# Kernel tuning notes

Hardware: AMD Instinct MI355X
Metric: run time of the kernel (lower is better)

## Reference

```python
import jax, jax.numpy as jnp
import numpy as np

EMBED_DIM = 1024
NUM_HEADS = 16
HEAD_DIM = EMBED_DIM // NUM_HEADS
SCALE = HEAD_DIM ** -0.5


def setup_inputs() -> dict:
    key = jax.random.key(0)
    ks = jax.random.split(key, 5)
    B, N, D = 2, 2048, EMBED_DIM
    std = D ** -0.5
    x = jax.random.normal(ks[0], (B, N, D), dtype=jnp.float32)
    W_qkv = jax.random.normal(ks[1], (D, 3 * D), dtype=jnp.float32) * std
    b_qkv = jnp.zeros((3 * D,), dtype=jnp.float32)
    W_proj = jax.random.normal(ks[2], (D, D), dtype=jnp.float32) * std
    b_proj = jnp.zeros((D,), dtype=jnp.float32)
    return {"x": x, "W_qkv": W_qkv, "b_qkv": b_qkv, "W_proj": W_proj, "b_proj": b_proj}


def reference(x, W_qkv, b_qkv, W_proj, b_proj):
    B, N, D = x.shape
    H, Hd = NUM_HEADS, HEAD_DIM
    qkv = x @ W_qkv + b_qkv                      # (B, N, 3D)
    qkv = qkv.reshape(B, N, 3, H, Hd)
    q = qkv[:, :, 0].transpose(0, 2, 1, 3)       # (B, H, N, Hd)
    k = qkv[:, :, 1].transpose(0, 2, 1, 3)
    v = qkv[:, :, 2].transpose(0, 2, 1, 3)
    attn = jnp.einsum('bhqd,bhkd->bhqk', q, k) * SCALE  # (B, H, N, N)
    attn = jax.nn.softmax(attn, axis=-1)
    out = jnp.einsum('bhqk,bhkd->bhqd', attn, v)        # (B, H, N, Hd)
    out = out.transpose(0, 2, 1, 3).reshape(B, N, D)
    return out @ W_proj + b_proj
```

## Files before the change

kernel.cpp:

```cpp
#include <hip/hip_runtime.h>
#include <stdint.h>

#define BATCH 2
#define NH 16
#define SEQ 2048
#define DIM 1024
#define HD 64
#define MROWS (BATCH*SEQ)

typedef __attribute__((ext_vector_type(8))) _Float16 f16x8;
typedef __attribute__((ext_vector_type(4))) _Float16 f16x4;
typedef __attribute__((ext_vector_type(2))) __fp16 fp16x2;
typedef __attribute__((ext_vector_type(4))) float f32x4;
typedef __attribute__((ext_vector_type(4))) short short4v;

__device__ __forceinline__ short f2h(float f) {
  union { _Float16 h; short s; } u;
  u.h = (_Float16)f;
  return u.s;
}

__device__ __forceinline__ float fast_exp2(float x) {
#if __has_builtin(__builtin_amdgcn_exp2f)
  return __builtin_amdgcn_exp2f(x);
#else
  return exp2f(x);
#endif
}

__device__ __forceinline__ f16x4 pack4(float p0, float p1, float p2, float p3) {
  union { struct { fp16x2 a, b; } p; f16x4 v; } u;
  u.p.a = __builtin_amdgcn_cvt_pkrtz(p0, p1);
  u.p.b = __builtin_amdgcn_cvt_pkrtz(p2, p3);
  return u.v;
}

__device__ __forceinline__ void async_load16(const void* g, void* l) {
  __builtin_amdgcn_global_load_lds((const __attribute__((address_space(1))) void*)g,
                                   (__attribute__((address_space(3))) void*)l, 16, 0, 0);
}

__global__ __launch_bounds__(256) void k_cvt(const float* __restrict__ in,
                                             short* __restrict__ out, int n4) {
  int i = blockIdx.x * 256 + threadIdx.x;
  if (i >= n4) return;
  float4 v = ((const float4*)in)[i];
  short4v o;
  o[0] = f2h(v.x); o[1] = f2h(v.y); o[2] = f2h(v.z); o[3] = f2h(v.w);
  ((short4v*)out)[i] = o;
}

__global__ __launch_bounds__(256) void k_transpose(const float* __restrict__ in,
                                                   short* __restrict__ out,
                                                   int K, int N) {
  __shared__ float t[32][33];
  int n0 = blockIdx.x * 32, k0 = blockIdx.y * 32;
  int tx = threadIdx.x, ty = threadIdx.y;
  #pragma unroll
  for (int i = 0; i < 32; i += 8)
    t[ty + i][tx] = in[(size_t)(k0 + ty + i) * N + (n0 + tx)];
  __syncthreads();
  #pragma unroll
  for (int i = 0; i < 32; i += 8)
    out[(size_t)(n0 + ty + i) * K + (k0 + tx)] = f2h(t[tx][ty + i]);
}

template <int MODE>
__global__ __launch_bounds__(256) void k_gemm_bt(
    const short* __restrict__ A, const short* __restrict__ Bt,
    const float* __restrict__ bias,
    short* __restrict__ Qd, short* __restrict__ Kd, short* __restrict__ Vtd,
    float* __restrict__ Cf, int Ncols, int Kdim) {
  constexpr int BM = 128, BN = 128, BK = 32;
  __shared__ short Al[BM * BK];
  __shared__ short Bl[BN * BK];
  const int tid = threadIdx.x;
  const int lane = tid & 63;
  const int wid = tid >> 6;
  const int wr = wid >> 1, wc = wid & 1;
  const int m0 = blockIdx.y * BM, n0 = blockIdx.x * BN;
  const int l15 = lane & 15, lk = (lane >> 4) * 8;

  f32x4 acc[4][4] = {};

  for (int k0 = 0; k0 < Kdim; k0 += BK) {
    __syncthreads();
    #pragma unroll
    for (int i = 0; i < 2; i++) {
      int c = i * 256 + tid;
      async_load16(A + (size_t)(m0 + (c >> 2)) * Kdim + k0 + (c & 3) * 8, &Al[c * 8]);
    }
    #pragma unroll
    for (int i = 0; i < 2; i++) {
      int c = i * 256 + tid;
      async_load16(Bt + (size_t)(n0 + (c >> 2)) * Kdim + k0 + (c & 3) * 8, &Bl[c * 8]);
    }
    __syncthreads();

    f16x8 af[4], bfr[4];
    #pragma unroll
    for (int i = 0; i < 4; i++)
      af[i] = *(const f16x8*)&Al[(wr * 64 + i * 16 + l15) * BK + lk];
    #pragma unroll
    for (int j = 0; j < 4; j++)
      bfr[j] = *(const f16x8*)&Bl[(wc * 64 + j * 16 + l15) * BK + lk];
    #pragma unroll
    for (int i = 0; i < 4; i++)
      #pragma unroll
      for (int j = 0; j < 4; j++)
        acc[i][j] = __builtin_amdgcn_mfma_f32_16x16x32_f16(af[i], bfr[j], acc[i][j], 0, 0, 0);
  }

  const int rl = (lane >> 4) * 4;
  if (MODE == 0) {
    #pragma unroll
    for (int j = 0; j < 4; j++) {
      int col = n0 + wc * 64 + j * 16 + l15;
      float bv = bias[col];
      int sec = col >> 10;
      int cc = col & 1023;
      int h = cc >> 6, hd = cc & 63;
      float mul = (sec == 0) ? (0.125f * 1.44269504088896f) : 1.0f;
      #pragma unroll
      for (int i = 0; i < 4; i++) {
        int rowb = m0 + wr * 64 + i * 16 + rl;
        #pragma unroll
        for (int r = 0; r < 4; r++) {
          int row = rowb + r;
          int b = row >> 11, nr = row & 2047;
          short v = f2h((acc[i][j][r] + bv) * mul);
          size_t bh = (size_t)(b * NH + h);
          if (sec == 0)      Qd[(bh * SEQ + nr) * HD + hd] = v;
          else if (sec == 1) Kd[(bh * SEQ + nr) * HD + hd] = v;
          else               Vtd[(bh * HD + hd) * SEQ + nr] = v;
        }
      }
    }
  } else {
    #pragma unroll
    for (int j = 0; j < 4; j++) {
      int col = n0 + wc * 64 + j * 16 + l15;
      float bv = bias[col];
      #pragma unroll
      for (int i = 0; i < 4; i++) {
        int rowb = m0 + wr * 64 + i * 16 + rl;
        #pragma unroll
        for (int r = 0; r < 4; r++)
          Cf[(size_t)(rowb + r) * Ncols + col] = acc[i][j][r] + bv;
      }
    }
  }
}

#define QBLK 64
#define KVBLK 64
#define PLD 72

__global__ __launch_bounds__(256) void k_flash(const short* __restrict__ Qd,
                                               const short* __restrict__ Kd,
                                               const short* __restrict__ Vtd,
                                               short* __restrict__ Od) {
  __shared__ short Kl[KVBLK * PLD];
  __shared__ short Vl[HD * PLD];
  __shared__ short Pl[4][16 * PLD];
  const int tid = threadIdx.x;
  const int lane = tid & 63;
  const int w = tid >> 6;
  const int l15 = lane & 15, g = lane >> 4;
  const int bh = blockIdx.y;
  const int q0 = blockIdx.x * QBLK + w * 16;
  const size_t base_qk = (size_t)bh * SEQ * HD;
  const size_t base_vt = (size_t)bh * HD * SEQ;

  f16x8 qf[2];
  #pragma unroll
  for (int s = 0; s < 2; s++)
    qf[s] = *(const f16x8*)(Qd + base_qk + (size_t)(q0 + l15) * HD + s * 32 + g * 8);

  f32x4 o[4] = {};
  float lsum = 0.f;

  for (int kv0 = 0; kv0 < SEQ; kv0 += KVBLK) {
    f16x8 kreg[2], vreg[2];
    #pragma unroll
    for (int i = 0; i < 2; i++) {
      int c = i * 256 + tid;
      kreg[i] = *(const f16x8*)(Kd + base_qk + (size_t)(kv0 + (c >> 3)) * HD + (c & 7) * 8);
      vreg[i] = *(const f16x8*)(Vtd + base_vt + (size_t)(c >> 3) * SEQ + kv0 + (c & 7) * 8);
    }
    __syncthreads();
    #pragma unroll
    for (int i = 0; i < 2; i++) {
      int c = i * 256 + tid;
      *(f16x8*)&Kl[(c >> 3) * PLD + (c & 7) * 8] = kreg[i];
      *(f16x8*)&Vl[(c >> 3) * PLD + (c & 7) * 8] = vreg[i];
    }
    __syncthreads();

    f32x4 s[4] = {};
    #pragma unroll
    for (int t = 0; t < 4; t++)
      #pragma unroll
      for (int ss = 0; ss < 2; ss++) {
        f16x8 kb = *(const f16x8*)&Kl[(t * 16 + l15) * PLD + ss * 32 + g * 8];
        s[t] = __builtin_amdgcn_mfma_f32_16x16x32_f16(kb, qf[ss], s[t], 0, 0, 0);
      }

    #pragma unroll
    for (int t = 0; t < 4; t++) {
      float p0 = fast_exp2(s[t][0]);
      float p1 = fast_exp2(s[t][1]);
      float p2 = fast_exp2(s[t][2]);
      float p3 = fast_exp2(s[t][3]);
      lsum += (p0 + p1) + (p2 + p3);
      *(f16x4*)&Pl[w][l15 * PLD + t * 16 + g * 4] = pack4(p0, p1, p2, p3);
    }
    asm volatile("s_waitcnt lgkmcnt(0)" ::: "memory");

    f16x8 pa[2];
    #pragma unroll
    for (int ks = 0; ks < 2; ks++)
      pa[ks] = *(const f16x8*)&Pl[w][l15 * PLD + ks * 32 + g * 8];
    #pragma unroll
    for (int t = 0; t < 4; t++)
      #pragma unroll
      for (int ks = 0; ks < 2; ks++) {
        f16x8 vb = *(const f16x8*)&Vl[(t * 16 + l15) * PLD + ks * 32 + g * 8];
        o[t] = __builtin_amdgcn_mfma_f32_16x16x32_f16(pa[ks], vb, o[t], 0, 0, 0);
      }
  }

  lsum += __shfl_xor(lsum, 16);
  lsum += __shfl_xor(lsum, 32);
  float inv = 1.f / lsum;
  float invr[4];
  #pragma unroll
  for (int r = 0; r < 4; r++)
    invr[r] = __shfl(inv, (g * 16) + (g * 4 + r));

  const int b = bh >> 4, h = bh & 15;
  #pragma unroll
  for (int t = 0; t < 4; t++)
    #pragma unroll
    for (int r = 0; r < 4; r++) {
      int q = q0 + g * 4 + r;
      Od[(size_t)(b * SEQ + q) * DIM + h * 64 + t * 16 + l15] = f2h(o[t][r] * invr[r]);
    }
}

extern "C" void kernel_launch(void* const* d_in, const int* in_sizes, int n_in,
                              void* d_out, int out_size, void* d_ws, size_t ws_size,
                              hipStream_t stream) {
  const float* x     = (const float*)d_in[0];
  const float* Wqkv  = (const float*)d_in[1];
  const float* bqkv  = (const float*)d_in[2];
  const float* Wproj = (const float*)d_in[3];
  const float* bproj = (const float*)d_in[4];
  float* out = (float*)d_out;

  char* ws = (char*)d_ws;
  short* x_h    = (short*)(ws);
  short* Wqkv_t = (short*)(ws + ((size_t)8  << 20));
  short* Wproj_t= (short*)(ws + ((size_t)14 << 20));
  short* Qd     = (short*)(ws + ((size_t)16 << 20));
  short* Kd     = (short*)(ws + ((size_t)24 << 20));
  short* Vtd    = (short*)(ws + ((size_t)32 << 20));
  short* Od     = (short*)(ws + ((size_t)40 << 20));

  k_cvt<<<(MROWS * DIM / 4 + 255) / 256, 256, 0, stream>>>(x, x_h, MROWS * DIM / 4);
  dim3 tb(32, 8);
  k_transpose<<<dim3(3 * DIM / 32, DIM / 32), tb, 0, stream>>>(Wqkv, Wqkv_t, DIM, 3 * DIM);
  k_transpose<<<dim3(DIM / 32, DIM / 32), tb, 0, stream>>>(Wproj, Wproj_t, DIM, DIM);
  k_gemm_bt<0><<<dim3(3 * DIM / 128, MROWS / 128), 256, 0, stream>>>(
      x_h, Wqkv_t, bqkv, Qd, Kd, Vtd, nullptr, 3 * DIM, DIM);
  k_flash<<<dim3(SEQ / QBLK, BATCH * NH), 256, 0, stream>>>(Qd, Kd, Vtd, Od);
  k_gemm_bt<1><<<dim3(DIM / 128, MROWS / 128), 256, 0, stream>>>(
      Od, Wproj_t, bproj, nullptr, nullptr, nullptr, out, DIM, DIM);
}
```

Baseline: 150.9 us.

## Double query rows per wave, swizzle LDS, and prefetch next KV tile

Each wave now handles 32 query rows instead of 16 (QBLK 128), so every K/V fragment read from LDS feeds two MFMAs. The padded LDS layout is replaced by an XOR swizzle to avoid bank conflicts. The KV loop is unrolled by two, and the global load of the next tile is issued before computing the current one to hide latency. s_setprio hints are added around the MFMA sections. The costs are higher register pressure and half as many blocks, which may reduce occupancy. The launch grid must also match the new QBLK.

```diff
diff --git a/kernel.cpp b/kernel.cpp
--- a/kernel.cpp
+++ b/kernel.cpp
@@ -152,91 +152,124 @@
   }
 }
 
-#define QBLK 64
+#define QBLK 128
 #define KVBLK 64
-#define PLD 72
+#define SWZ(r, cs) (((r) * 64 + (cs)) ^ (((r) & 7) << 3))
 
 __global__ __launch_bounds__(256) void k_flash(const short* __restrict__ Qd,
                                                const short* __restrict__ Kd,
                                                const short* __restrict__ Vtd,
                                                short* __restrict__ Od) {
-  __shared__ short Kl[KVBLK * PLD];
-  __shared__ short Vl[HD * PLD];
-  __shared__ short Pl[4][16 * PLD];
+  __shared__ short Kl[KVBLK * 64];
+  __shared__ short Vl[HD * 64];
+  __shared__ short Pl[4][32 * 64];
   const int tid = threadIdx.x;
   const int lane = tid & 63;
   const int w = tid >> 6;
   const int l15 = lane & 15, g = lane >> 4;
   const int bh = blockIdx.y;
-  const int q0 = blockIdx.x * QBLK + w * 16;
+  const int q0 = blockIdx.x * QBLK + w * 32;
   const size_t base_qk = (size_t)bh * SEQ * HD;
   const size_t base_vt = (size_t)bh * HD * SEQ;
-
-  f16x8 qf[2];
-  #pragma unroll
-  for (int s = 0; s < 2; s++)
-    qf[s] = *(const f16x8*)(Qd + base_qk + (size_t)(q0 + l15) * HD + s * 32 + g * 8);
-
-  f32x4 o[4] = {};
-  float lsum = 0.f;
-
-  for (int kv0 = 0; kv0 < SEQ; kv0 += KVBLK) {
-    f16x8 kreg[2], vreg[2];
-    #pragma unroll
-    for (int i = 0; i < 2; i++) {
-      int c = i * 256 + tid;
-      kreg[i] = *(const f16x8*)(Kd + base_qk + (size_t)(kv0 + (c >> 3)) * HD + (c & 7) * 8);
-      vreg[i] = *(const f16x8*)(Vtd + base_vt + (size_t)(c >> 3) * SEQ + kv0 + (c & 7) * 8);
-    }
-    __syncthreads();
-    #pragma unroll
-    for (int i = 0; i < 2; i++) {
-      int c = i * 256 + tid;
-      *(f16x8*)&Kl[(c >> 3) * PLD + (c & 7) * 8] = kreg[i];
-      *(f16x8*)&Vl[(c >> 3) * PLD + (c & 7) * 8] = vreg[i];
-    }
-    __syncthreads();
-
-    f32x4 s[4] = {};
+  const short* Kbase = Kd + base_qk;
+  const short* Vbase = Vtd + base_vt;
+
+  f16x8 qf0[2], qf1[2];
+  #pragma unroll
+  for (int ss = 0; ss < 2; ss++) {
+    qf0[ss] = *(const f16x8*)(Qd + base_qk + (size_t)(q0 + l15) * HD + ss * 32 + g * 8);
+    qf1[ss] = *(const f16x8*)(Qd + base_qk + (size_t)(q0 + 16 + l15) * HD + ss * 32 + g * 8);
+  }
+
+  f32x4 o0[4] = {}, o1[4] = {};
+  float lsum0 = 0.f, lsum1 = 0.f;
+
+  const int srow = tid >> 3;
+  const int scol = (tid & 7) * 8;
+
+#define LOADKV(kv, kr, vr) do {                                                  \
+    kr[0] = *(const f16x8*)(Kbase + (size_t)((kv) + srow) * HD + scol);          \
+    kr[1] = *(const f16x8*)(Kbase + (size_t)((kv) + 32 + srow) * HD + scol);     \
+    vr[0] = *(const f16x8*)(Vbase + (size_t)srow * SEQ + (kv) + scol);           \
+    vr[1] = *(const f16x8*)(Vbase + (size_t)(32 + srow) * SEQ + (kv) + scol);    \
+  } while (0)
+
+#define STOREKV(kr, vr) do {                                                     \
+    *(f16x8*)&Kl[SWZ(srow, scol)] = kr[0];                                       \
+    *(f16x8*)&Kl[SWZ(32 + srow, scol)] = kr[1];                                  \
+    *(f16x8*)&Vl[SWZ(srow, scol)] = vr[0];                                       \
+    *(f16x8*)&Vl[SWZ(32 + srow, scol)] = vr[1];                                  \
+  } while (0)
+
+  auto compute = [&]() {
+    f32x4 s0[4] = {}, s1[4] = {};
+    __builtin_amdgcn_s_setprio(1);
     #pragma unroll
     for (int t = 0; t < 4; t++)
       #pragma unroll
       for (int ss = 0; ss < 2; ss++) {
-        f16x8 kb = *(const f16x8*)&Kl[(t * 16 + l15) * PLD + ss * 32 + g * 8];
-        s[t] = __builtin_amdgcn_mfma_f32_16x16x32_f16(kb, qf[ss], s[t], 0, 0, 0);
+        f16x8 kb = *(const f16x8*)&Kl[SWZ(t * 16 + l15, ss * 32 + g * 8)];
+        s0[t] = __builtin_amdgcn_mfma_f32_16x16x32_f16(kb, qf0[ss], s0[t], 0, 0, 0);
+        s1[t] = __builtin_amdgcn_mfma_f32_16x16x32_f16(kb, qf1[ss], s1[t], 0, 0, 0);
       }
-
+    __builtin_amdgcn_s_setprio(0);
     #pragma unroll
     for (int t = 0; t < 4; t++) {
-      float p0 = fast_exp2(s[t][0]);
-      float p1 = fast_exp2(s[t][1]);
-      float p2 = fast_exp2(s[t][2]);
-      float p3 = fast_exp2(s[t][3]);
-      lsum += (p0 + p1) + (p2 + p3);
-      *(f16x4*)&Pl[w][l15 * PLD + t * 16 + g * 4] = pack4(p0, p1, p2, p3);
+      float a0 = fast_exp2(s0[t][0]), a1 = fast_exp2(s0[t][1]);
+      float a2 = fast_exp2(s0[t][2]), a3 = fast_exp2(s0[t][3]);
+      lsum0 += (a0 + a1) + (a2 + a3);
+      *(f16x4*)&Pl[w][SWZ(l15, t * 16 + g * 4)] = pack4(a0, a1, a2, a3);
+      float b0 = fast_exp2(s1[t][0]), b1 = fast_exp2(s1[t][1]);
+      float b2 = fast_exp2(s1[t][2]), b3 = fast_exp2(s1[t][3]);
+      lsum1 += (b0 + b1) + (b2 + b3);
+      *(f16x4*)&Pl[w][SWZ(16 + l15, t * 16 + g * 4)] = pack4(b0, b1, b2, b3);
     }
     asm volatile("s_waitcnt lgkmcnt(0)" ::: "memory");
-
-    f16x8 pa[2];
-    #pragma unroll
-    for (int ks = 0; ks < 2; ks++)
-      pa[ks] = *(const f16x8*)&Pl[w][l15 * PLD + ks * 32 + g * 8];
+    f16x8 pa0[2], pa1[2];
+    #pragma unroll
+    for (int ks = 0; ks < 2; ks++) {
+      pa0[ks] = *(const f16x8*)&Pl[w][SWZ(l15, ks * 32 + g * 8)];
+      pa1[ks] = *(const f16x8*)&Pl[w][SWZ(16 + l15, ks * 32 + g * 8)];
+    }
+    __builtin_amdgcn_s_setprio(1);
     #pragma unroll
     for (int t = 0; t < 4; t++)
       #pragma unroll
       for (int ks = 0; ks < 2; ks++) {
-        f16x8 vb = *(const f16x8*)&Vl[(t * 16 + l15) * PLD + ks * 32 + g * 8];
-        o[t] = __builtin_amdgcn_mfma_f32_16x16x32_f16(pa[ks], vb, o[t], 0, 0, 0);
+        f16x8 vb = *(const f16x8*)&Vl[SWZ(t * 16 + l15, ks * 32 + g * 8)];
+        o0[t] = __builtin_amdgcn_mfma_f32_16x16x32_f16(pa0[ks], vb, o0[t], 0, 0, 0);
+        o1[t] = __builtin_amdgcn_mfma_f32_16x16x32_f16(pa1[ks], vb, o1[t], 0, 0, 0);
       }
-  }
-
-  lsum += __shfl_xor(lsum, 16);
-  lsum += __shfl_xor(lsum, 32);
-  float inv = 1.f / lsum;
-  float invr[4];
-  #pragma unroll
-  for (int r = 0; r < 4; r++)
-    invr[r] = __shfl(inv, (g * 16) + (g * 4 + r));
+    __builtin_amdgcn_s_setprio(0);
+  };
+
+  f16x8 ka[2], va[2], kb2[2], vb2[2];
+  LOADKV(0, ka, va);
+  for (int kv0 = 0; kv0 < SEQ; kv0 += 2 * KVBLK) {
+    __syncthreads();
+    STOREKV(ka, va);
+    __syncthreads();
+    LOADKV(kv0 + KVBLK, kb2, vb2);
+    compute();
+    __syncthreads();
+    STOREKV(kb2, vb2);
+    __syncthreads();
+    int nxt = kv0 + 2 * KVBLK;
+    if (nxt < SEQ) LOADKV(nxt, ka, va);
+    compute();
+  }
+
+  lsum0 += __shfl_xor(lsum0, 16);
+  lsum0 += __shfl_xor(lsum0, 32);
+  lsum1 += __shfl_xor(lsum1, 16);
+  lsum1 += __shfl_xor(lsum1, 32);
+  float inv0 = 1.f / lsum0, inv1 = 1.f / lsum1;
+  float invr0[4], invr1[4];
+  #pragma unroll
+  for (int r = 0; r < 4; r++) {
+    invr0[r] = __shfl(inv0, g * 16 + g * 4 + r);
+    invr1[r] = __shfl(inv1, g * 16 + g * 4 + r);
+  }
 
   const int b = bh >> 4, h = bh & 15;
   #pragma unroll
@@ -244,8 +277,11 @@
     #pragma unroll
     for (int r = 0; r < 4; r++) {
       int q = q0 + g * 4 + r;
-      Od[(size_t)(b * SEQ + q) * DIM + h * 64 + t * 16 + l15] = f2h(o[t][r] * invr[r]);
-    }
+      Od[(size_t)(b * SEQ + q) * DIM + h * 64 + t * 16 + l15] = f2h(o0[t][r] * invr0[r]);
+      Od[(size_t)(b * SEQ + q + 16) * DIM + h * 64 + t * 16 + l15] = f2h(o1[t][r] * invr1[r]);
+    }
+#undef LOADKV
+#undef STOREKV
 }
 
 extern "C" void kernel_launch(void* const* d_in, const int* in_sizes, int n_in,
```

Result: faster. 138.6 us (-8.1%).

## Restructure flash attention with 32x32 MFMA, pre-swizzled K/V and async double buffering

Applied to the files above, without the earlier changes.

The QKV GEMM epilogue now writes K and V in a pre-swizzled, MFMA-fragment-ordered layout, so the flash kernel can stream each 64-key tile into LDS with async global-to-LDS loads into a double buffer. The flash kernel moves to 32x32x16 MFMAs with 64 query rows per wave (256 per block). P is kept in registers via lane permutes instead of a round trip through LDS, and the grid is reordered so blocks sharing a head run together. This aims to cut LDS traffic, global load latency and sync stalls, at the cost of higher register pressure, fewer blocks, and scattered 2-byte stores in the GEMM epilogue.

```diff
diff --git a/kernel.cpp b/kernel.cpp
--- a/kernel.cpp
+++ b/kernel.cpp
@@ -9,9 +9,9 @@
 #define MROWS (BATCH*SEQ)
 
 typedef __attribute__((ext_vector_type(8))) _Float16 f16x8;
-typedef __attribute__((ext_vector_type(4))) _Float16 f16x4;
+typedef __attribute__((ext_vector_type(16))) float f32x16;
+typedef __attribute__((ext_vector_type(4))) float f32x4;
 typedef __attribute__((ext_vector_type(2))) __fp16 fp16x2;
-typedef __attribute__((ext_vector_type(4))) float f32x4;
 typedef __attribute__((ext_vector_type(4))) short short4v;
 
 __device__ __forceinline__ short f2h(float f) {
@@ -28,11 +28,19 @@
 #endif
 }
 
-__device__ __forceinline__ f16x4 pack4(float p0, float p1, float p2, float p3) {
-  union { struct { fp16x2 a, b; } p; f16x4 v; } u;
-  u.p.a = __builtin_amdgcn_cvt_pkrtz(p0, p1);
-  u.p.b = __builtin_amdgcn_cvt_pkrtz(p2, p3);
-  return u.v;
+__device__ __forceinline__ unsigned pk2(float a, float b) {
+  union { fp16x2 h; unsigned u; } x;
+  x.h = __builtin_amdgcn_cvt_pkrtz(a, b);
+  return x.u;
+}
+
+__device__ __forceinline__ void perm32swap(unsigned &a, unsigned &b) {
+  unsigned as = (unsigned)__shfl_xor((int)a, 32);
+  unsigned bs = (unsigned)__shfl_xor((int)b, 32);
+  bool lo = ((threadIdx.x & 63) < 32);
+  unsigned na = lo ? a : bs;
+  unsigned nb = lo ? as : b;
+  a = na; b = nb;
 }
 
 __device__ __forceinline__ void async_load16(const void* g, void* l) {
@@ -130,9 +138,16 @@
           int b = row >> 11, nr = row & 2047;
           short v = f2h((acc[i][j][r] + bv) * mul);
           size_t bh = (size_t)(b * NH + h);
-          if (sec == 0)      Qd[(bh * SEQ + nr) * HD + hd] = v;
-          else if (sec == 1) Kd[(bh * SEQ + nr) * HD + hd] = v;
-          else               Vtd[(bh * HD + hd) * SEQ + nr] = v;
+          size_t base2 = bh * (size_t)(SEQ * HD);
+          if (sec == 0) {
+            Qd[base2 + (size_t)nr * HD + hd] = v;
+          } else if (sec == 1) {
+            Kd[base2 + (size_t)(((nr >> 5) * 4 + (hd >> 4)) * 512 +
+                                (((hd >> 3) & 1) * 32 + (nr & 31)) * 8 + (hd & 7))] = v;
+          } else {
+            Vtd[base2 + (size_t)(((nr >> 4) * 2 + (hd >> 5)) * 512 +
+                                 (((nr >> 3) & 1) * 32 + (hd & 31)) * 8 + (nr & 7))] = v;
+          }
         }
       }
     }
@@ -152,100 +167,130 @@
   }
 }
 
-#define QBLK 64
-#define KVBLK 64
-#define PLD 72
+#define QBLK 256
+#define NKVT (SEQ / 64)
+
+#define PACK8(sv, R0, lsv, OUT) do {                                        \
+    float e0_ = fast_exp2((sv)[R0 + 0]), e1_ = fast_exp2((sv)[R0 + 1]);     \
+    float e2_ = fast_exp2((sv)[R0 + 2]), e3_ = fast_exp2((sv)[R0 + 3]);     \
+    float e4_ = fast_exp2((sv)[R0 + 4]), e5_ = fast_exp2((sv)[R0 + 5]);     \
+    float e6_ = fast_exp2((sv)[R0 + 6]), e7_ = fast_exp2((sv)[R0 + 7]);     \
+    lsv += ((e0_ + e1_) + (e2_ + e3_)) + ((e4_ + e5_) + (e6_ + e7_));       \
+    unsigned u0_ = pk2(e0_, e1_), u1_ = pk2(e2_, e3_);                      \
+    unsigned u2_ = pk2(e4_, e5_), u3_ = pk2(e6_, e7_);                      \
+    perm32swap(u0_, u2_);                                                   \
+    perm32swap(u1_, u3_);                                                   \
+    union { unsigned u[4]; f16x8 v; } W_;                                   \
+    W_.u[0] = u0_; W_.u[1] = u1_; W_.u[2] = u2_; W_.u[3] = u3_;             \
+    OUT = W_.v;                                                             \
+  } while (0)
 
 __global__ __launch_bounds__(256) void k_flash(const short* __restrict__ Qd,
-                                               const short* __restrict__ Kd,
-                                               const short* __restrict__ Vtd,
+                                               const short* __restrict__ KB,
+                                               const short* __restrict__ VB,
                                                short* __restrict__ Od) {
-  __shared__ short Kl[KVBLK * PLD];
-  __shared__ short Vl[HD * PLD];
-  __shared__ short Pl[4][16 * PLD];
+  __shared__ short Kl[2][4096];
+  __shared__ short Vl[2][4096];
   const int tid = threadIdx.x;
   const int lane = tid & 63;
   const int w = tid >> 6;
-  const int l15 = lane & 15, g = lane >> 4;
-  const int bh = blockIdx.y;
-  const int q0 = blockIdx.x * QBLK + w * 16;
-  const size_t base_qk = (size_t)bh * SEQ * HD;
-  const size_t base_vt = (size_t)bh * HD * SEQ;
-
-  f16x8 qf[2];
+  const int l31 = lane & 31, lh = lane >> 5;
+  const int bh = blockIdx.x;
+  const int q0 = blockIdx.y * QBLK + w * 64;
+  const size_t base = (size_t)bh * (size_t)(SEQ * HD);
+
+  f16x8 qf[2][4];
   #pragma unroll
-  for (int s = 0; s < 2; s++)
-    qf[s] = *(const f16x8*)(Qd + base_qk + (size_t)(q0 + l15) * HD + s * 32 + g * 8);
-
-  f32x4 o[4] = {};
-  float lsum = 0.f;
-
-  for (int kv0 = 0; kv0 < SEQ; kv0 += KVBLK) {
-    f16x8 kreg[2], vreg[2];
-    #pragma unroll
-    for (int i = 0; i < 2; i++) {
-      int c = i * 256 + tid;
-      kreg[i] = *(const f16x8*)(Kd + base_qk + (size_t)(kv0 + (c >> 3)) * HD + (c & 7) * 8);
-      vreg[i] = *(const f16x8*)(Vtd + base_vt + (size_t)(c >> 3) * SEQ + kv0 + (c & 7) * 8);
-    }
+  for (int qt = 0; qt < 2; qt++)
+    #pragma unroll
+    for (int ds = 0; ds < 4; ds++)
+      qf[qt][ds] = *(const f16x8*)(Qd + base + (size_t)(q0 + qt * 32 + l31) * HD +
+                                   ds * 16 + lh * 8);
+
+  f32x16 o[2][2] = {};
+  float lsum0 = 0.f, lsum1 = 0.f;
+
+#define STAGE(kvt, buf) do {                                                \
+    const short* ks_ = KB + base + (size_t)(kvt) * 4096;                    \
+    const short* vs_ = VB + base + (size_t)(kvt) * 4096;                    \
+    async_load16(ks_ + tid * 8, &Kl[buf][tid * 8]);                         \
+    async_load16(ks_ + (tid + 256) * 8, &Kl[buf][(tid + 256) * 8]);         \
+    async_load16(vs_ + tid * 8, &Vl[buf][tid * 8]);                         \
+    async_load16(vs_ + (tid + 256) * 8, &Vl[buf][(tid + 256) * 8]);         \
+  } while (0)
+
+  auto compute = [&](int cur) {
+    f16x8 p0[4], p1[4];
+    {
+      f16x8 kf[4];
+      #pragma unroll
+      for (int ds = 0; ds < 4; ds++)
+        kf[ds] = *(const f16x8*)&Kl[cur][(ds * 64 + lane) * 8];
+      f32x16 sA0 = {}, sA1 = {};
+      #pragma unroll
+      for (int ds = 0; ds < 4; ds++) {
+        sA0 = __builtin_amdgcn_mfma_f32_32x32x16_f16(kf[ds], qf[0][ds], sA0, 0, 0, 0);
+        sA1 = __builtin_amdgcn_mfma_f32_32x32x16_f16(kf[ds], qf[1][ds], sA1, 0, 0, 0);
+      }
+      PACK8(sA0, 0, lsum0, p0[0]); PACK8(sA0, 8, lsum0, p0[1]);
+      PACK8(sA1, 0, lsum1, p1[0]); PACK8(sA1, 8, lsum1, p1[1]);
+    }
+    {
+      f16x8 kf[4];
+      #pragma unroll
+      for (int ds = 0; ds < 4; ds++)
+        kf[ds] = *(const f16x8*)&Kl[cur][((4 + ds) * 64 + lane) * 8];
+      f32x16 sB0 = {}, sB1 = {};
+      #pragma unroll
+      for (int ds = 0; ds < 4; ds++) {
+        sB0 = __builtin_amdgcn_mfma_f32_32x32x16_f16(kf[ds], qf[0][ds], sB0, 0, 0, 0);
+        sB1 = __builtin_amdgcn_mfma_f32_32x32x16_f16(kf[ds], qf[1][ds], sB1, 0, 0, 0);
+      }
+      PACK8(sB0, 0, lsum0, p0[2]); PACK8(sB0, 8, lsum0, p0[3]);
+      PACK8(sB1, 0, lsum1, p1[2]); PACK8(sB1, 8, lsum1, p1[3]);
+    }
+    f16x8 vf[4][2];
+    #pragma unroll
+    for (int ks = 0; ks < 4; ks++)
+      #pragma unroll
+      for (int hdt = 0; hdt < 2; hdt++)
+        vf[ks][hdt] = *(const f16x8*)&Vl[cur][((ks * 2 + hdt) * 64 + lane) * 8];
+    #pragma unroll
+    for (int ks = 0; ks < 4; ks++) {
+      o[0][0] = __builtin_amdgcn_mfma_f32_32x32x16_f16(p0[ks], vf[ks][0], o[0][0], 0, 0, 0);
+      o[0][1] = __builtin_amdgcn_mfma_f32_32x32x16_f16(p0[ks], vf[ks][1], o[0][1], 0, 0, 0);
+      o[1][0] = __builtin_amdgcn_mfma_f32_32x32x16_f16(p1[ks], vf[ks][0], o[1][0], 0, 0, 0);
+      o[1][1] = __builtin_amdgcn_mfma_f32_32x32x16_f16(p1[ks], vf[ks][1], o[1][1], 0, 0, 0);
+    }
+  };
+
+  STAGE(0, 0);
+  __syncthreads();
+  for (int kvt = 0; kvt < NKVT; kvt++) {
+    int cur = kvt & 1;
+    if (kvt + 1 < NKVT) STAGE(kvt + 1, cur ^ 1);
+    compute(cur);
     __syncthreads();
-    #pragma unroll
-    for (int i = 0; i < 2; i++) {
-      int c = i * 256 + tid;
-      *(f16x8*)&Kl[(c >> 3) * PLD + (c & 7) * 8] = kreg[i];
-      *(f16x8*)&Vl[(c >> 3) * PLD + (c & 7) * 8] = vreg[i];
-    }
-    __syncthreads();
-
-    f32x4 s[4] = {};
-    #pragma unroll
-    for (int t = 0; t < 4; t++)
-      #pragma unroll
-      for (int ss = 0; ss < 2; ss++) {
-        f16x8 kb = *(const f16x8*)&Kl[(t * 16 + l15) * PLD + ss * 32 + g * 8];
-        s[t] = __builtin_amdgcn_mfma_f32_16x16x32_f16(kb, qf[ss], s[t], 0, 0, 0);
-      }
-
-    #pragma unroll
-    for (int t = 0; t < 4; t++) {
-      float p0 = fast_exp2(s[t][0]);
-      float p1 = fast_exp2(s[t][1]);
-      float p2 = fast_exp2(s[t][2]);
-      float p3 = fast_exp2(s[t][3]);
-      lsum += (p0 + p1) + (p2 + p3);
-      *(f16x4*)&Pl[w][l15 * PLD + t * 16 + g * 4] = pack4(p0, p1, p2, p3);
-    }
-    asm volatile("s_waitcnt lgkmcnt(0)" ::: "memory");
-
-    f16x8 pa[2];
-    #pragma unroll
-    for (int ks = 0; ks < 2; ks++)
-      pa[ks] = *(const f16x8*)&Pl[w][l15 * PLD + ks * 32 + g * 8];
-    #pragma unroll
-    for (int t = 0; t < 4; t++)
-      #pragma unroll
-      for (int ks = 0; ks < 2; ks++) {
-        f16x8 vb = *(const f16x8*)&Vl[(t * 16 + l15) * PLD + ks * 32 + g * 8];
-        o[t] = __builtin_amdgcn_mfma_f32_16x16x32_f16(pa[ks], vb, o[t], 0, 0, 0);
-      }
   }
-
-  lsum += __shfl_xor(lsum, 16);
-  lsum += __shfl_xor(lsum, 32);
-  float inv = 1.f / lsum;
-  float invr[4];
-  #pragma unroll
-  for (int r = 0; r < 4; r++)
-    invr[r] = __shfl(inv, (g * 16) + (g * 4 + r));
+#undef STAGE
+
+  lsum0 += __shfl_xor(lsum0, 32);
+  lsum1 += __shfl_xor(lsum1, 32);
+  float inv0 = 1.f / lsum0, inv1 = 1.f / lsum1;
 
   const int b = bh >> 4, h = bh & 15;
   #pragma unroll
-  for (int t = 0; t < 4; t++)
-    #pragma unroll
-    for (int r = 0; r < 4; r++) {
-      int q = q0 + g * 4 + r;
-      Od[(size_t)(b * SEQ + q) * DIM + h * 64 + t * 16 + l15] = f2h(o[t][r] * invr[r]);
-    }
+  for (int reg = 0; reg < 16; reg++) {
+    int qrow = (reg & 3) + 8 * (reg >> 2) + 4 * lh;
+    float s0 = __shfl(inv0, qrow);
+    float s1 = __shfl(inv1, qrow);
+    size_t r0 = (size_t)(b * SEQ + q0 + qrow) * DIM + h * 64;
+    size_t r1 = (size_t)(b * SEQ + q0 + 32 + qrow) * DIM + h * 64;
+    Od[r0 + l31]      = f2h(o[0][0][reg] * s0);
+    Od[r0 + 32 + l31] = f2h(o[0][1][reg] * s0);
+    Od[r1 + l31]      = f2h(o[1][0][reg] * s1);
+    Od[r1 + 32 + l31] = f2h(o[1][1][reg] * s1);
+  }
 }
 
 extern "C" void kernel_launch(void* const* d_in, const int* in_sizes, int n_in,
@@ -273,7 +318,7 @@
   k_transpose<<<dim3(DIM / 32, DIM / 32), tb, 0, stream>>>(Wproj, Wproj_t, DIM, DIM);
   k_gemm_bt<0><<<dim3(3 * DIM / 128, MROWS / 128), 256, 0, stream>>>(
       x_h, Wqkv_t, bqkv, Qd, Kd, Vtd, nullptr, 3 * DIM, DIM);
-  k_flash<<<dim3(SEQ / QBLK, BATCH * NH), 256, 0, stream>>>(Qd, Kd, Vtd, Od);
+  k_flash<<<dim3(BATCH * NH, SEQ / QBLK), 256, 0, stream>>>(Qd, Kd, Vtd, Od);
   k_gemm_bt<1><<<dim3(DIM / 128, MROWS / 128), 256, 0, stream>>>(
       Od, Wproj_t, bproj, nullptr, nullptr, nullptr, out, DIM, DIM);
 }
```

After: 161.9 us. 7.3% more time.
